# Kernel optimization log

Hardware: AMD Instinct MI355X
Metric: run time of the kernel (lower is better)

## Reference

```python
import jax, jax.numpy as jnp
import numpy as np

N = 100000      # num_nodes
E = 1600000     # num_edges (avg degree 16)
D_IN, D_H, D_OUT = 128, 128, 64


def _glorot(key, shape):
    fan_in = shape[0]
    bound = 1.0 / np.sqrt(fan_in)
    return jax.random.uniform(key, shape, jnp.float32, -bound, bound)


def setup_inputs() -> dict:
    key = jax.random.key(0)
    ks = jax.random.split(key, 9)
    x = jax.random.normal(ks[0], (N, D_IN), jnp.float32)
    edge_index = jax.random.randint(ks[1], (2, E), 0, N, jnp.int32)
    # SAGEConv layer 1: lin_l (aggregated, with bias) and lin_r (root, no bias)
    W1l = _glorot(ks[2], (D_IN, D_H))
    b1 = jnp.zeros((D_H,), jnp.float32)
    W1r = _glorot(ks[3], (D_IN, D_H))
    # SAGEConv layer 2
    W2l = _glorot(ks[4], (D_H, D_OUT))
    b2 = jnp.zeros((D_OUT,), jnp.float32)
    W2r = _glorot(ks[5], (D_H, D_OUT))
    return {"x": x, "W1l": W1l, "b1": b1, "W1r": W1r,
            "W2l": W2l, "b2": b2, "W2r": W2r, "edge_index": edge_index}


def _sage_conv(x, edge_index, Wl, b, Wr):
    """PyG SAGEConv with mean aggregation: out = mean_{j in N(i)} x_j @ Wl + b + x_i @ Wr."""
    src, dst = edge_index[0], edge_index[1]
    msg_sum = jax.ops.segment_sum(x[src], dst, num_segments=N)          # [N, d_in]
    deg = jax.ops.segment_sum(jnp.ones((src.shape[0],), x.dtype), dst,
                              num_segments=N)                            # [N]
    mean = msg_sum / jnp.maximum(deg, 1.0)[:, None]
    return mean @ Wl + b + x @ Wr


def reference(x, W1l, b1, W1r, W2l, b2, W2r, edge_index):
    h = jax.nn.relu(_sage_conv(x, edge_index, W1l, b1, W1r))
    # dropout is identity at inference (training=False)
    return _sage_conv(h, edge_index, W2l, b2, W2r)
```

## Files before the change

kernel.cpp:

```cpp
#include <hip/hip_runtime.h>

#define NODES 100000
#define NEDGE 1600000
#define NPART 8
#define PSIZE (NODES / NPART)
#define EW 48

typedef _Float16 half8 __attribute__((ext_vector_type(8)));
typedef float floatx4 __attribute__((ext_vector_type(4)));
typedef float floatx2 __attribute__((ext_vector_type(2)));


static __device__ __forceinline__ unsigned int packh2(float a, float b) {
    union { _Float16 h; unsigned short s; } x, y;
    x.h = (_Float16)a; y.h = (_Float16)b;
    return (unsigned int)x.s | ((unsigned int)y.s << 16);
}
static __device__ __forceinline__ float2 unpackh2(unsigned int u) {
    union { unsigned short s; _Float16 h; } x, y;
    x.s = (unsigned short)(u & 0xffffu);
    y.s = (unsigned short)(u >> 16);
    return make_float2((float)x.h, (float)y.h);
}


template <bool HI>
static __device__ __forceinline__ float2 fp8x2_to_f32(unsigned int u) {
    floatx2 r = __builtin_amdgcn_cvt_pk_f32_fp8(u, HI);
    return make_float2(r.x, r.y);
}
static __device__ __forceinline__ unsigned int pack4fp8(float a, float b,
                                                        float c, float d) {
    unsigned int w = (unsigned int)__builtin_amdgcn_cvt_pk_fp8_f32(a, b, 0, false);
    w = (unsigned int)__builtin_amdgcn_cvt_pk_fp8_f32(c, d, (int)w, true);
    return w;
}


static __global__ __launch_bounds__(256) void prep_kernel(
    const float* __restrict__ W1l, const float* __restrict__ W1r,
    const float* __restrict__ W2l, const float* __restrict__ W2r,
    _Float16* __restrict__ WT1, _Float16* __restrict__ WT2,
    int* __restrict__ cnt) {
    int bid = blockIdx.x;
    if (bid < 192) {
        int idx = bid * 256 + threadIdx.x;
        if (idx < 256 * 128) {
            int n = idx >> 7, k = idx & 127;
            float v = (n < 128) ? W1l[k * 128 + n] : W1r[k * 128 + (n - 128)];
            WT1[n * 128 + k] = (_Float16)v;
        } else if (idx < 256 * 128 + 128 * 128) {
            int i2 = idx - 256 * 128;
            int n = i2 >> 7, k = i2 & 127;
            float v = (n < 64) ? W2l[k * 64 + n] : W2r[k * 64 + (n - 64)];
            WT2[n * 128 + k] = (_Float16)v;
        }
    } else {
        int i = (bid - 192) * 256 + threadIdx.x;
        int stride = 128 * 256;
        for (; i < NODES; i += stride) cnt[i] = 0;
    }
}


static __global__ __launch_bounds__(256) void build_ell_kernel(
    const int* __restrict__ src, const int* __restrict__ dst,
    int* __restrict__ cnt, int* __restrict__ colE,
    int ebase, int eend) {
    const int part = blockIdx.x & (NPART - 1);
    const int lo = part * PSIZE;
    const int hi = lo + PSIZE;
    const int group = blockIdx.x >> 3;
    const int ngroups = gridDim.x >> 3;
    int i = group * 256 + threadIdx.x;
    int stride = ngroups * 256;
    for (int e = ebase + i; e < eend; e += stride) {
        int d = __builtin_nontemporal_load(dst + e);
        if (d >= lo && d < hi) {
            int sv = __builtin_nontemporal_load(src + e);
            int pos = atomicAdd(&cnt[d], 1);
            if (pos < EW) colE[(size_t)d * EW + pos] = sv;
        }
    }
}


static __global__ __launch_bounds__(256) void gemm1_mfma_kernel(
    const float* __restrict__ X, const _Float16* __restrict__ WT1,
    const float* __restrict__ b1,
    unsigned char* __restrict__ U8, _Float16* __restrict__ V16) {
    __shared__ _Float16 sX[64][136];
    const int tid = threadIdx.x;
    const int row0 = blockIdx.x * 64;
    {
        int c4 = (tid & 31) * 4;
        int r0 = tid >> 5;
#pragma unroll
        for (int p = 0; p < 8; ++p) {
            int r = r0 + p * 8;
            int row = row0 + r;
            float4 v = make_float4(0.f, 0.f, 0.f, 0.f);
            if (row < NODES) v = *(const float4*)(X + (size_t)row * 128 + c4);
            uint2 o;
            o.x = packh2(v.x, v.y);
            o.y = packh2(v.z, v.w);
            *(uint2*)&sX[r][c4] = o;
        }
    }
    __syncthreads();

    const int wave = tid >> 6;
    const int lane = tid & 63;
    const int l15 = lane & 15;
    const int quad = lane >> 4;

    floatx4 acc[4][4];
#pragma unroll
    for (int j = 0; j < 4; ++j)
#pragma unroll
        for (int m = 0; m < 4; ++m) acc[j][m] = (floatx4){0.f, 0.f, 0.f, 0.f};

    const _Float16* Wbase = WT1 + (size_t)(wave * 64 + l15) * 128 + quad * 8;

    for (int k0 = 0; k0 < 128; k0 += 32) {
        half8 a[4];
#pragma unroll
        for (int m = 0; m < 4; ++m)
            a[m] = *(const half8*)&sX[m * 16 + l15][quad * 8 + k0];
#pragma unroll
        for (int j = 0; j < 4; ++j) {
            half8 b = *(const half8*)(Wbase + (size_t)j * 16 * 128 + k0);
#pragma unroll
            for (int m = 0; m < 4; ++m)
                acc[j][m] = __builtin_amdgcn_mfma_f32_16x16x32_f16(b, a[m], acc[j][m], 0, 0, 0);
        }
    }

    if (wave < 2) {
#pragma unroll
        for (int j = 0; j < 4; ++j) {
            int n0 = wave * 64 + j * 16 + quad * 4;
#pragma unroll
            for (int m = 0; m < 4; ++m) {
                int node = row0 + m * 16 + l15;
                if (node < NODES) {
                    unsigned int w = pack4fp8(acc[j][m][0], acc[j][m][1],
                                              acc[j][m][2], acc[j][m][3]);
                    *(unsigned int*)(U8 + (size_t)node * 128 + n0) = w;
                }
            }
        }
    } else {
#pragma unroll
        for (int j = 0; j < 4; ++j) {
            int nn0 = (wave - 2) * 64 + j * 16 + quad * 4;
            float4 bb = *(const float4*)(b1 + nn0);
#pragma unroll
            for (int m = 0; m < 4; ++m) {
                int node = row0 + m * 16 + l15;
                if (node < NODES) {
                    uint2 o;
                    o.x = packh2(acc[j][m][0] + bb.x, acc[j][m][1] + bb.y);
                    o.y = packh2(acc[j][m][2] + bb.z, acc[j][m][3] + bb.w);
                    *(uint2*)(V16 + (size_t)node * 128 + nn0) = o;
                }
            }
        }
    }
}


static __global__ __launch_bounds__(256) void agg1_kernel(
    const unsigned char* __restrict__ U8, const int* __restrict__ cnt,
    const int* __restrict__ colE, unsigned int* __restrict__ H32) {
    int node = (int)((blockIdx.x * 256 + threadIdx.x) >> 6);
    int lane = threadIdx.x & 63;
    if (node >= NODES) return;
    const int g = lane >> 4;
    const int l16 = lane & 15;
    int dcnt = cnt[node];
    if (dcnt > EW) dcnt = EW;
    int s = node * EW;
    int e = s + dcnt;
    float inv = 1.0f / (float)max(dcnt, 1);

    float acc[8];
#pragma unroll
    for (int i = 0; i < 8; ++i) acc[i] = 0.f;

    int p = s + g;
    for (; p + 12 < e; p += 16) {
        int c0 = colE[p], c1 = colE[p + 4], c2 = colE[p + 8], c3 = colE[p + 12];
        uint2 u0 = *(const uint2*)(U8 + (size_t)c0 * 128 + l16 * 8);
        uint2 u1 = *(const uint2*)(U8 + (size_t)c1 * 128 + l16 * 8);
        uint2 u2 = *(const uint2*)(U8 + (size_t)c2 * 128 + l16 * 8);
        uint2 u3 = *(const uint2*)(U8 + (size_t)c3 * 128 + l16 * 8);
#pragma unroll
        for (int q = 0; q < 4; ++q) {
            uint2 u = (q == 0) ? u0 : (q == 1) ? u1 : (q == 2) ? u2 : u3;
            float2 a0 = fp8x2_to_f32<false>(u.x), a1 = fp8x2_to_f32<true>(u.x);
            float2 a2 = fp8x2_to_f32<false>(u.y), a3 = fp8x2_to_f32<true>(u.y);
            acc[0] += a0.x; acc[1] += a0.y; acc[2] += a1.x; acc[3] += a1.y;
            acc[4] += a2.x; acc[5] += a2.y; acc[6] += a3.x; acc[7] += a3.y;
        }
    }
    for (; p < e; p += 4) {
        uint2 u = *(const uint2*)(U8 + (size_t)colE[p] * 128 + l16 * 8);
        float2 a0 = fp8x2_to_f32<false>(u.x), a1 = fp8x2_to_f32<true>(u.x);
        float2 a2 = fp8x2_to_f32<false>(u.y), a3 = fp8x2_to_f32<true>(u.y);
        acc[0] += a0.x; acc[1] += a0.y; acc[2] += a1.x; acc[3] += a1.y;
        acc[4] += a2.x; acc[5] += a2.y; acc[6] += a3.x; acc[7] += a3.y;
    }

#pragma unroll
    for (int i = 0; i < 8; ++i) {
        acc[i] += __shfl_xor(acc[i], 16);
        acc[i] += __shfl_xor(acc[i], 32);
    }

    if (lane < 16) {
        uint4 vv = *(const uint4*)(H32 + (size_t)node * 64 + l16 * 4);
        float2 v0 = unpackh2(vv.x), v1 = unpackh2(vv.y);
        float2 v2 = unpackh2(vv.z), v3 = unpackh2(vv.w);
        uint4 o;
        o.x = packh2(fmaxf(acc[0] * inv + v0.x, 0.f), fmaxf(acc[1] * inv + v0.y, 0.f));
        o.y = packh2(fmaxf(acc[2] * inv + v1.x, 0.f), fmaxf(acc[3] * inv + v1.y, 0.f));
        o.z = packh2(fmaxf(acc[4] * inv + v2.x, 0.f), fmaxf(acc[5] * inv + v2.y, 0.f));
        o.w = packh2(fmaxf(acc[6] * inv + v3.x, 0.f), fmaxf(acc[7] * inv + v3.y, 0.f));
        *(uint4*)(H32 + (size_t)node * 64 + l16 * 4) = o;
    }
}


static __global__ __launch_bounds__(256) void gemm2_mfma_kernel(
    const _Float16* __restrict__ H16, const _Float16* __restrict__ WT2,
    const float* __restrict__ b2,
    _Float16* __restrict__ T16, float* __restrict__ OUT) {
    __shared__ _Float16 sX[64][136];
    const int tid = threadIdx.x;
    const int row0 = blockIdx.x * 64;
    {
        int c8 = (tid & 15) * 8;
        int r0 = tid >> 4;
#pragma unroll
        for (int p = 0; p < 4; ++p) {
            int r = r0 + p * 16;
            int row = row0 + r;
            uint4 v = make_uint4(0u, 0u, 0u, 0u);
            if (row < NODES) v = *(const uint4*)(H16 + (size_t)row * 128 + c8);
            *(uint4*)&sX[r][c8] = v;
        }
    }
    __syncthreads();

    const int wave = tid >> 6;
    const int lane = tid & 63;
    const int l15 = lane & 15;
    const int quad = lane >> 4;

    floatx4 acc[2][4];
#pragma unroll
    for (int j = 0; j < 2; ++j)
#pragma unroll
        for (int m = 0; m < 4; ++m) acc[j][m] = (floatx4){0.f, 0.f, 0.f, 0.f};

    const _Float16* Wbase = WT2 + (size_t)(wave * 32 + l15) * 128 + quad * 8;

    for (int k0 = 0; k0 < 128; k0 += 32) {
        half8 a[4];
#pragma unroll
        for (int m = 0; m < 4; ++m)
            a[m] = *(const half8*)&sX[m * 16 + l15][quad * 8 + k0];
#pragma unroll
        for (int j = 0; j < 2; ++j) {
            half8 b = *(const half8*)(Wbase + (size_t)j * 16 * 128 + k0);
#pragma unroll
            for (int m = 0; m < 4; ++m)
                acc[j][m] = __builtin_amdgcn_mfma_f32_16x16x32_f16(b, a[m], acc[j][m], 0, 0, 0);
        }
    }

    const bool isOut = (wave >= 2);
#pragma unroll
    for (int j = 0; j < 2; ++j) {
        int n0 = wave * 32 + j * 16 + quad * 4;
        if (isOut) {
            int nn0 = n0 - 64;
            float4 bb = *(const float4*)(b2 + nn0);
#pragma unroll
            for (int m = 0; m < 4; ++m) {
                int node = row0 + m * 16 + l15;
                if (node < NODES) {
                    float4 o = make_float4(acc[j][m][0] + bb.x, acc[j][m][1] + bb.y,
                                           acc[j][m][2] + bb.z, acc[j][m][3] + bb.w);
                    *(float4*)(OUT + (size_t)node * 64 + nn0) = o;
                }
            }
        } else {
#pragma unroll
            for (int m = 0; m < 4; ++m) {
                int node = row0 + m * 16 + l15;
                if (node < NODES) {
                    uint2 o;
                    o.x = packh2(acc[j][m][0], acc[j][m][1]);
                    o.y = packh2(acc[j][m][2], acc[j][m][3]);
                    *(uint2*)(T16 + (size_t)node * 64 + n0) = o;
                }
            }
        }
    }
}


static __global__ __launch_bounds__(256) void agg2_kernel(
    const unsigned int* __restrict__ T32, const int* __restrict__ cnt,
    const int* __restrict__ colE, float* __restrict__ OUT) {
    int node = (int)((blockIdx.x * 256 + threadIdx.x) >> 6);
    int lane = threadIdx.x & 63;
    if (node >= NODES) return;
    const int g = lane >> 4;
    const int l16 = lane & 15;
    int dcnt = cnt[node];
    if (dcnt > EW) dcnt = EW;
    int s = node * EW;
    int e = s + dcnt;
    float inv = 1.0f / (float)max(dcnt, 1);

    float acc[4];
#pragma unroll
    for (int i = 0; i < 4; ++i) acc[i] = 0.f;

    int p = s + g;
    for (; p + 12 < e; p += 16) {
        int c0 = colE[p], c1 = colE[p + 4], c2 = colE[p + 8], c3 = colE[p + 12];
        uint2 u0 = *(const uint2*)(T32 + (size_t)c0 * 32 + l16 * 2);
        uint2 u1 = *(const uint2*)(T32 + (size_t)c1 * 32 + l16 * 2);
        uint2 u2 = *(const uint2*)(T32 + (size_t)c2 * 32 + l16 * 2);
        uint2 u3 = *(const uint2*)(T32 + (size_t)c3 * 32 + l16 * 2);
#pragma unroll
        for (int q = 0; q < 4; ++q) {
            uint2 u = (q == 0) ? u0 : (q == 1) ? u1 : (q == 2) ? u2 : u3;
            float2 a0 = unpackh2(u.x), a1 = unpackh2(u.y);
            acc[0] += a0.x; acc[1] += a0.y; acc[2] += a1.x; acc[3] += a1.y;
        }
    }
    for (; p < e; p += 4) {
        uint2 u = *(const uint2*)(T32 + (size_t)colE[p] * 32 + l16 * 2);
        float2 a0 = unpackh2(u.x), a1 = unpackh2(u.y);
        acc[0] += a0.x; acc[1] += a0.y; acc[2] += a1.x; acc[3] += a1.y;
    }

#pragma unroll
    for (int i = 0; i < 4; ++i) {
        acc[i] += __shfl_xor(acc[i], 16);
        acc[i] += __shfl_xor(acc[i], 32);
    }

    if (lane < 16) {
        float4 o = *(float4*)(OUT + (size_t)node * 64 + l16 * 4);
        o.x += acc[0] * inv;
        o.y += acc[1] * inv;
        o.z += acc[2] * inv;
        o.w += acc[3] * inv;
        *(float4*)(OUT + (size_t)node * 64 + l16 * 4) = o;
    }
}


extern "C" void kernel_launch(void* const* d_in, const int* in_sizes, int n_in,
                              void* d_out, int out_size, void* d_ws, size_t ws_size,
                              hipStream_t stream) {
    const float* x   = (const float*)d_in[0];
    const float* W1l = (const float*)d_in[1];
    const float* b1  = (const float*)d_in[2];
    const float* W1r = (const float*)d_in[3];
    const float* W2l = (const float*)d_in[4];
    const float* b2  = (const float*)d_in[5];
    const float* W2r = (const float*)d_in[6];
    const int*   ei  = (const int*)d_in[7];
    const int* esrc = ei;
    const int* edst = ei + NEDGE;
    float* out = (float*)d_out;

    char* ws = (char*)d_ws;
    size_t off = 0;
    int* colE     = (int*)(ws + off); off += (size_t)NODES * EW * 4;
    unsigned char* U8 = (unsigned char*)(ws + off); off += (size_t)NODES * 128;
    _Float16* V16 = (_Float16*)(ws + off); off += (size_t)NODES * 128 * 2;
    int* cnt      = (int*)(ws + off); off += (((size_t)NODES * 4) + 255) & ~(size_t)255;
    _Float16* WT1 = (_Float16*)(ws + off); off += 256 * 128 * 2;
    _Float16* WT2 = (_Float16*)(ws + off); off += 128 * 128 * 2;
    _Float16* T16 = (_Float16*)U8;

    const int gemm_grid = (NODES + 63) / 64;
    const int agg_grid  = (NODES + 3) / 4;

    prep_kernel<<<320, 256, 0, stream>>>(W1l, W1r, W2l, W2r, WT1, WT2, cnt);
    build_ell_kernel<<<1024, 256, 0, stream>>>(esrc, edst, cnt, colE,
                                               0, NEDGE / 2);
    build_ell_kernel<<<1024, 256, 0, stream>>>(esrc, edst, cnt, colE,
                                               NEDGE / 2, NEDGE);

    gemm1_mfma_kernel<<<gemm_grid, 256, 0, stream>>>(x, WT1, b1, U8, V16);
    agg1_kernel<<<agg_grid, 256, 0, stream>>>(U8, cnt, colE, (unsigned int*)V16);

    gemm2_mfma_kernel<<<gemm_grid, 256, 0, stream>>>(V16, WT2, b2, T16, out);
    agg2_kernel<<<agg_grid, 256, 0, stream>>>(
        (const unsigned int*)T16, cnt, colE, out);
}
```

Baseline: 372.0 us.

## Fuse layer-1 aggregation into layer-2 GEMM and merge ELL build launches

Layer-1 mean aggregation (with root add and ReLU) now runs inside the layer-2 MFMA GEMM block. Each wave aggregates 16 nodes straight into shared memory instead of writing H to global and reading it back. T16 is written into the V16 buffer with a 128-half stride, and agg2 indexing is updated to match. The two half-range ELL build launches become a single 2048-block launch. Fusing drops one global round trip and one launch, but each GEMM block now serialises 16 gather loops per wave, which lowers memory-level parallelism compared with one wave per node across the whole grid.

```diff
diff --git a/kernel.cpp b/kernel.cpp
--- a/kernel.cpp
+++ b/kernel.cpp
@@ -65,8 +65,7 @@
 
 static __global__ __launch_bounds__(256) void build_ell_kernel(
     const int* __restrict__ src, const int* __restrict__ dst,
-    int* __restrict__ cnt, int* __restrict__ colE,
-    int ebase, int eend) {
+    int* __restrict__ cnt, int* __restrict__ colE) {
     const int part = blockIdx.x & (NPART - 1);
     const int lo = part * PSIZE;
     const int hi = lo + PSIZE;
@@ -74,7 +73,7 @@
     const int ngroups = gridDim.x >> 3;
     int i = group * 256 + threadIdx.x;
     int stride = ngroups * 256;
-    for (int e = ebase + i; e < eend; e += stride) {
+    for (int e = i; e < NEDGE; e += stride) {
         int d = __builtin_nontemporal_load(dst + e);
         if (d >= lo && d < hi) {
             int sv = __builtin_nontemporal_load(src + e);
@@ -170,99 +169,86 @@
 }
 
 
-static __global__ __launch_bounds__(256) void agg1_kernel(
+static __global__ __launch_bounds__(256) void agg1_gemm2_kernel(
     const unsigned char* __restrict__ U8, const int* __restrict__ cnt,
-    const int* __restrict__ colE, unsigned int* __restrict__ H32) {
-    int node = (int)((blockIdx.x * 256 + threadIdx.x) >> 6);
-    int lane = threadIdx.x & 63;
-    if (node >= NODES) return;
-    const int g = lane >> 4;
-    const int l16 = lane & 15;
-    int dcnt = cnt[node];
-    if (dcnt > EW) dcnt = EW;
-    int s = node * EW;
-    int e = s + dcnt;
-    float inv = 1.0f / (float)max(dcnt, 1);
-
-    float acc[8];
-#pragma unroll
-    for (int i = 0; i < 8; ++i) acc[i] = 0.f;
-
-    int p = s + g;
-    for (; p + 12 < e; p += 16) {
-        int c0 = colE[p], c1 = colE[p + 4], c2 = colE[p + 8], c3 = colE[p + 12];
-        uint2 u0 = *(const uint2*)(U8 + (size_t)c0 * 128 + l16 * 8);
-        uint2 u1 = *(const uint2*)(U8 + (size_t)c1 * 128 + l16 * 8);
-        uint2 u2 = *(const uint2*)(U8 + (size_t)c2 * 128 + l16 * 8);
-        uint2 u3 = *(const uint2*)(U8 + (size_t)c3 * 128 + l16 * 8);
-#pragma unroll
-        for (int q = 0; q < 4; ++q) {
-            uint2 u = (q == 0) ? u0 : (q == 1) ? u1 : (q == 2) ? u2 : u3;
-            float2 a0 = fp8x2_to_f32<false>(u.x), a1 = fp8x2_to_f32<true>(u.x);
-            float2 a2 = fp8x2_to_f32<false>(u.y), a3 = fp8x2_to_f32<true>(u.y);
-            acc[0] += a0.x; acc[1] += a0.y; acc[2] += a1.x; acc[3] += a1.y;
-            acc[4] += a2.x; acc[5] += a2.y; acc[6] += a3.x; acc[7] += a3.y;
-        }
-    }
-    for (; p < e; p += 4) {
-        uint2 u = *(const uint2*)(U8 + (size_t)colE[p] * 128 + l16 * 8);
-        float2 a0 = fp8x2_to_f32<false>(u.x), a1 = fp8x2_to_f32<true>(u.x);
-        float2 a2 = fp8x2_to_f32<false>(u.y), a3 = fp8x2_to_f32<true>(u.y);
-        acc[0] += a0.x; acc[1] += a0.y; acc[2] += a1.x; acc[3] += a1.y;
-        acc[4] += a2.x; acc[5] += a2.y; acc[6] += a3.x; acc[7] += a3.y;
-    }
-
-#pragma unroll
-    for (int i = 0; i < 8; ++i) {
-        acc[i] += __shfl_xor(acc[i], 16);
-        acc[i] += __shfl_xor(acc[i], 32);
-    }
-
-    if (lane < 16) {
-        uint4 vv = *(const uint4*)(H32 + (size_t)node * 64 + l16 * 4);
-        float2 v0 = unpackh2(vv.x), v1 = unpackh2(vv.y);
-        float2 v2 = unpackh2(vv.z), v3 = unpackh2(vv.w);
-        uint4 o;
-        o.x = packh2(fmaxf(acc[0] * inv + v0.x, 0.f), fmaxf(acc[1] * inv + v0.y, 0.f));
-        o.y = packh2(fmaxf(acc[2] * inv + v1.x, 0.f), fmaxf(acc[3] * inv + v1.y, 0.f));
-        o.z = packh2(fmaxf(acc[4] * inv + v2.x, 0.f), fmaxf(acc[5] * inv + v2.y, 0.f));
-        o.w = packh2(fmaxf(acc[6] * inv + v3.x, 0.f), fmaxf(acc[7] * inv + v3.y, 0.f));
-        *(uint4*)(H32 + (size_t)node * 64 + l16 * 4) = o;
-    }
-}
-
-
-static __global__ __launch_bounds__(256) void gemm2_mfma_kernel(
-    const _Float16* __restrict__ H16, const _Float16* __restrict__ WT2,
-    const float* __restrict__ b2,
-    _Float16* __restrict__ T16, float* __restrict__ OUT) {
+    const int* __restrict__ colE, const _Float16* __restrict__ WT2,
+    const float* __restrict__ b2, _Float16* __restrict__ V16,
+    float* __restrict__ OUT) {
     __shared__ _Float16 sX[64][136];
     const int tid = threadIdx.x;
     const int row0 = blockIdx.x * 64;
-    {
-        int c8 = (tid & 15) * 8;
-        int r0 = tid >> 4;
-#pragma unroll
-        for (int p = 0; p < 4; ++p) {
-            int r = r0 + p * 16;
-            int row = row0 + r;
-            uint4 v = make_uint4(0u, 0u, 0u, 0u);
-            if (row < NODES) v = *(const uint4*)(H16 + (size_t)row * 128 + c8);
-            *(uint4*)&sX[r][c8] = v;
-        }
-    }
-    __syncthreads();
-
     const int wave = tid >> 6;
     const int lane = tid & 63;
+    const int g = lane >> 4;
+    const int l16 = lane & 15;
+    const unsigned int* H32 = (const unsigned int*)V16;
+
+    for (int m = 0; m < 16; ++m) {
+        const int r = wave * 16 + m;
+        const int node = row0 + r;
+        float acc[8];
+#pragma unroll
+        for (int i = 0; i < 8; ++i) acc[i] = 0.f;
+        float inv = 1.0f;
+        if (node < NODES) {
+            int dcnt = cnt[node];
+            if (dcnt > EW) dcnt = EW;
+            int s = node * EW;
+            int e = s + dcnt;
+            inv = 1.0f / (float)max(dcnt, 1);
+            int p = s + g;
+            for (; p + 12 < e; p += 16) {
+                int c0 = colE[p], c1 = colE[p + 4], c2 = colE[p + 8], c3 = colE[p + 12];
+                uint2 u0 = *(const uint2*)(U8 + (size_t)c0 * 128 + l16 * 8);
+                uint2 u1 = *(const uint2*)(U8 + (size_t)c1 * 128 + l16 * 8);
+                uint2 u2 = *(const uint2*)(U8 + (size_t)c2 * 128 + l16 * 8);
+                uint2 u3 = *(const uint2*)(U8 + (size_t)c3 * 128 + l16 * 8);
+#pragma unroll
+                for (int q = 0; q < 4; ++q) {
+                    uint2 u = (q == 0) ? u0 : (q == 1) ? u1 : (q == 2) ? u2 : u3;
+                    float2 a0 = fp8x2_to_f32<false>(u.x), a1 = fp8x2_to_f32<true>(u.x);
+                    float2 a2 = fp8x2_to_f32<false>(u.y), a3 = fp8x2_to_f32<true>(u.y);
+                    acc[0] += a0.x; acc[1] += a0.y; acc[2] += a1.x; acc[3] += a1.y;
+                    acc[4] += a2.x; acc[5] += a2.y; acc[6] += a3.x; acc[7] += a3.y;
+                }
+            }
+            for (; p < e; p += 4) {
+                uint2 u = *(const uint2*)(U8 + (size_t)colE[p] * 128 + l16 * 8);
+                float2 a0 = fp8x2_to_f32<false>(u.x), a1 = fp8x2_to_f32<true>(u.x);
+                float2 a2 = fp8x2_to_f32<false>(u.y), a3 = fp8x2_to_f32<true>(u.y);
+                acc[0] += a0.x; acc[1] += a0.y; acc[2] += a1.x; acc[3] += a1.y;
+                acc[4] += a2.x; acc[5] += a2.y; acc[6] += a3.x; acc[7] += a3.y;
+            }
+        }
+#pragma unroll
+        for (int i = 0; i < 8; ++i) {
+            acc[i] += __shfl_xor(acc[i], 16);
+            acc[i] += __shfl_xor(acc[i], 32);
+        }
+        if (lane < 16) {
+            uint4 o = make_uint4(0u, 0u, 0u, 0u);
+            if (node < NODES) {
+                uint4 vv = *(const uint4*)(H32 + (size_t)node * 64 + l16 * 4);
+                float2 v0 = unpackh2(vv.x), v1 = unpackh2(vv.y);
+                float2 v2 = unpackh2(vv.z), v3 = unpackh2(vv.w);
+                o.x = packh2(fmaxf(acc[0] * inv + v0.x, 0.f), fmaxf(acc[1] * inv + v0.y, 0.f));
+                o.y = packh2(fmaxf(acc[2] * inv + v1.x, 0.f), fmaxf(acc[3] * inv + v1.y, 0.f));
+                o.z = packh2(fmaxf(acc[4] * inv + v2.x, 0.f), fmaxf(acc[5] * inv + v2.y, 0.f));
+                o.w = packh2(fmaxf(acc[6] * inv + v3.x, 0.f), fmaxf(acc[7] * inv + v3.y, 0.f));
+            }
+            *(uint4*)&sX[r][l16 * 8] = o;
+        }
+    }
+    __syncthreads();
+
     const int l15 = lane & 15;
     const int quad = lane >> 4;
 
-    floatx4 acc[2][4];
+    floatx4 acc2[2][4];
 #pragma unroll
     for (int j = 0; j < 2; ++j)
 #pragma unroll
-        for (int m = 0; m < 4; ++m) acc[j][m] = (floatx4){0.f, 0.f, 0.f, 0.f};
+        for (int m = 0; m < 4; ++m) acc2[j][m] = (floatx4){0.f, 0.f, 0.f, 0.f};
 
     const _Float16* Wbase = WT2 + (size_t)(wave * 32 + l15) * 128 + quad * 8;
 
@@ -276,7 +262,7 @@
             half8 b = *(const half8*)(Wbase + (size_t)j * 16 * 128 + k0);
 #pragma unroll
             for (int m = 0; m < 4; ++m)
-                acc[j][m] = __builtin_amdgcn_mfma_f32_16x16x32_f16(b, a[m], acc[j][m], 0, 0, 0);
+                acc2[j][m] = __builtin_amdgcn_mfma_f32_16x16x32_f16(b, a[m], acc2[j][m], 0, 0, 0);
         }
     }
 
@@ -291,8 +277,8 @@
             for (int m = 0; m < 4; ++m) {
                 int node = row0 + m * 16 + l15;
                 if (node < NODES) {
-                    float4 o = make_float4(acc[j][m][0] + bb.x, acc[j][m][1] + bb.y,
-                                           acc[j][m][2] + bb.z, acc[j][m][3] + bb.w);
+                    float4 o = make_float4(acc2[j][m][0] + bb.x, acc2[j][m][1] + bb.y,
+                                           acc2[j][m][2] + bb.z, acc2[j][m][3] + bb.w);
                     *(float4*)(OUT + (size_t)node * 64 + nn0) = o;
                 }
             }
@@ -302,9 +288,9 @@
                 int node = row0 + m * 16 + l15;
                 if (node < NODES) {
                     uint2 o;
-                    o.x = packh2(acc[j][m][0], acc[j][m][1]);
-                    o.y = packh2(acc[j][m][2], acc[j][m][3]);
-                    *(uint2*)(T16 + (size_t)node * 64 + n0) = o;
+                    o.x = packh2(acc2[j][m][0], acc2[j][m][1]);
+                    o.y = packh2(acc2[j][m][2], acc2[j][m][3]);
+                    *(uint2*)(V16 + (size_t)node * 128 + n0) = o;
                 }
             }
         }
@@ -333,10 +319,10 @@
     int p = s + g;
     for (; p + 12 < e; p += 16) {
         int c0 = colE[p], c1 = colE[p + 4], c2 = colE[p + 8], c3 = colE[p + 12];
-        uint2 u0 = *(const uint2*)(T32 + (size_t)c0 * 32 + l16 * 2);
-        uint2 u1 = *(const uint2*)(T32 + (size_t)c1 * 32 + l16 * 2);
-        uint2 u2 = *(const uint2*)(T32 + (size_t)c2 * 32 + l16 * 2);
-        uint2 u3 = *(const uint2*)(T32 + (size_t)c3 * 32 + l16 * 2);
+        uint2 u0 = *(const uint2*)(T32 + (size_t)c0 * 64 + l16 * 2);
+        uint2 u1 = *(const uint2*)(T32 + (size_t)c1 * 64 + l16 * 2);
+        uint2 u2 = *(const uint2*)(T32 + (size_t)c2 * 64 + l16 * 2);
+        uint2 u3 = *(const uint2*)(T32 + (size_t)c3 * 64 + l16 * 2);
 #pragma unroll
         for (int q = 0; q < 4; ++q) {
             uint2 u = (q == 0) ? u0 : (q == 1) ? u1 : (q == 2) ? u2 : u3;
@@ -345,7 +331,7 @@
         }
     }
     for (; p < e; p += 4) {
-        uint2 u = *(const uint2*)(T32 + (size_t)colE[p] * 32 + l16 * 2);
+        uint2 u = *(const uint2*)(T32 + (size_t)colE[p] * 64 + l16 * 2);
         float2 a0 = unpackh2(u.x), a1 = unpackh2(u.y);
         acc[0] += a0.x; acc[1] += a0.y; acc[2] += a1.x; acc[3] += a1.y;
     }
@@ -390,21 +376,18 @@
     int* cnt      = (int*)(ws + off); off += (((size_t)NODES * 4) + 255) & ~(size_t)255;
     _Float16* WT1 = (_Float16*)(ws + off); off += 256 * 128 * 2;
     _Float16* WT2 = (_Float16*)(ws + off); off += 128 * 128 * 2;
-    _Float16* T16 = (_Float16*)U8;
 
     const int gemm_grid = (NODES + 63) / 64;
     const int agg_grid  = (NODES + 3) / 4;
 
     prep_kernel<<<320, 256, 0, stream>>>(W1l, W1r, W2l, W2r, WT1, WT2, cnt);
-    build_ell_kernel<<<1024, 256, 0, stream>>>(esrc, edst, cnt, colE,
-                                               0, NEDGE / 2);
-    build_ell_kernel<<<1024, 256, 0, stream>>>(esrc, edst, cnt, colE,
-                                               NEDGE / 2, NEDGE);
+    build_ell_kernel<<<2048, 256, 0, stream>>>(esrc, edst, cnt, colE);
 
     gemm1_mfma_kernel<<<gemm_grid, 256, 0, stream>>>(x, WT1, b1, U8, V16);
-    agg1_kernel<<<agg_grid, 256, 0, stream>>>(U8, cnt, colE, (unsigned int*)V16);
-
-    gemm2_mfma_kernel<<<gemm_grid, 256, 0, stream>>>(V16, WT2, b2, T16, out);
+
+    agg1_gemm2_kernel<<<gemm_grid, 256, 0, stream>>>(U8, cnt, colE, WT2, b2,
+                                                     V16, out);
+
     agg2_kernel<<<agg_grid, 256, 0, stream>>>(
-        (const unsigned int*)T16, cnt, colE, out);
-}
+        (const unsigned int*)V16, cnt, colE, out);
+}
```

Result: no change. 378.2 us (+1.7%).

## Process two nodes per wavefront in aggregation and merge ELL build launches

Applied to the files above, without the earlier changes.

Both aggregation kernels now give each 64-lane wavefront two destination nodes. Each iteration issues eight predicated gathers, four per node, with masked loads replacing the remainder loop, so more memory requests are in flight per wave. The ELL build collapses two half-range launches into a single launch with twice the blocks, removing one kernel launch. The cost is more registers per thread, wasted lanes when the two nodes' degrees differ, and a dummy row-0 load for each invalid slot.

```diff
diff --git a/kernel.cpp b/kernel.cpp
--- a/kernel.cpp
+++ b/kernel.cpp
@@ -65,8 +65,7 @@
 
 static __global__ __launch_bounds__(256) void build_ell_kernel(
     const int* __restrict__ src, const int* __restrict__ dst,
-    int* __restrict__ cnt, int* __restrict__ colE,
-    int ebase, int eend) {
+    int* __restrict__ cnt, int* __restrict__ colE) {
     const int part = blockIdx.x & (NPART - 1);
     const int lo = part * PSIZE;
     const int hi = lo + PSIZE;
@@ -74,7 +73,7 @@
     const int ngroups = gridDim.x >> 3;
     int i = group * 256 + threadIdx.x;
     int stride = ngroups * 256;
-    for (int e = ebase + i; e < eend; e += stride) {
+    for (int e = i; e < NEDGE; e += stride) {
         int d = __builtin_nontemporal_load(dst + e);
         if (d >= lo && d < hi) {
             int sv = __builtin_nontemporal_load(src + e);
@@ -173,61 +172,100 @@
 static __global__ __launch_bounds__(256) void agg1_kernel(
     const unsigned char* __restrict__ U8, const int* __restrict__ cnt,
     const int* __restrict__ colE, unsigned int* __restrict__ H32) {
-    int node = (int)((blockIdx.x * 256 + threadIdx.x) >> 6);
+    int pid = (int)((blockIdx.x * 256 + threadIdx.x) >> 6);
     int lane = threadIdx.x & 63;
-    if (node >= NODES) return;
+    const int nA = pid * 2;
+    const int nB = nA + 1;
+    if (nA >= NODES) return;
     const int g = lane >> 4;
     const int l16 = lane & 15;
-    int dcnt = cnt[node];
-    if (dcnt > EW) dcnt = EW;
-    int s = node * EW;
-    int e = s + dcnt;
-    float inv = 1.0f / (float)max(dcnt, 1);
-
-    float acc[8];
-#pragma unroll
-    for (int i = 0; i < 8; ++i) acc[i] = 0.f;
-
-    int p = s + g;
-    for (; p + 12 < e; p += 16) {
-        int c0 = colE[p], c1 = colE[p + 4], c2 = colE[p + 8], c3 = colE[p + 12];
-        uint2 u0 = *(const uint2*)(U8 + (size_t)c0 * 128 + l16 * 8);
-        uint2 u1 = *(const uint2*)(U8 + (size_t)c1 * 128 + l16 * 8);
-        uint2 u2 = *(const uint2*)(U8 + (size_t)c2 * 128 + l16 * 8);
-        uint2 u3 = *(const uint2*)(U8 + (size_t)c3 * 128 + l16 * 8);
+
+    int dA = cnt[nA]; if (dA > EW) dA = EW;
+    int dB = (nB < NODES) ? cnt[nB] : 0; if (dB > EW) dB = EW;
+    const int sA = nA * EW, sB = nB * EW;
+    const int eA = sA + dA, eB = sB + dB;
+    const float invA = 1.0f / (float)max(dA, 1);
+    const float invB = 1.0f / (float)max(dB, 1);
+    const int dmax = max(dA, dB);
+
+    float accA[8], accB[8];
+#pragma unroll
+    for (int i = 0; i < 8; ++i) { accA[i] = 0.f; accB[i] = 0.f; }
+
+    for (int t = 0; t * 16 < dmax; ++t) {
+        int bA = sA + g + t * 16, bB = sB + g + t * 16;
+        int pA0 = bA, pA1 = bA + 4, pA2 = bA + 8, pA3 = bA + 12;
+        int pB0 = bB, pB1 = bB + 4, pB2 = bB + 8, pB3 = bB + 12;
+        bool vA0 = pA0 < eA, vA1 = pA1 < eA, vA2 = pA2 < eA, vA3 = pA3 < eA;
+        bool vB0 = pB0 < eB, vB1 = pB1 < eB, vB2 = pB2 < eB, vB3 = pB3 < eB;
+        int cA0 = colE[vA0 ? pA0 : sA], cA1 = colE[vA1 ? pA1 : sA];
+        int cA2 = colE[vA2 ? pA2 : sA], cA3 = colE[vA3 ? pA3 : sA];
+        int cB0 = colE[vB0 ? pB0 : sB], cB1 = colE[vB1 ? pB1 : sB];
+        int cB2 = colE[vB2 ? pB2 : sB], cB3 = colE[vB3 ? pB3 : sB];
+        cA0 = vA0 ? cA0 : 0; cA1 = vA1 ? cA1 : 0;
+        cA2 = vA2 ? cA2 : 0; cA3 = vA3 ? cA3 : 0;
+        cB0 = vB0 ? cB0 : 0; cB1 = vB1 ? cB1 : 0;
+        cB2 = vB2 ? cB2 : 0; cB3 = vB3 ? cB3 : 0;
+        uint2 uA0 = *(const uint2*)(U8 + (size_t)cA0 * 128 + l16 * 8);
+        uint2 uA1 = *(const uint2*)(U8 + (size_t)cA1 * 128 + l16 * 8);
+        uint2 uA2 = *(const uint2*)(U8 + (size_t)cA2 * 128 + l16 * 8);
+        uint2 uA3 = *(const uint2*)(U8 + (size_t)cA3 * 128 + l16 * 8);
+        uint2 uB0 = *(const uint2*)(U8 + (size_t)cB0 * 128 + l16 * 8);
+        uint2 uB1 = *(const uint2*)(U8 + (size_t)cB1 * 128 + l16 * 8);
+        uint2 uB2 = *(const uint2*)(U8 + (size_t)cB2 * 128 + l16 * 8);
+        uint2 uB3 = *(const uint2*)(U8 + (size_t)cB3 * 128 + l16 * 8);
+        if (!vA0) { uA0.x = 0u; uA0.y = 0u; }
+        if (!vA1) { uA1.x = 0u; uA1.y = 0u; }
+        if (!vA2) { uA2.x = 0u; uA2.y = 0u; }
+        if (!vA3) { uA3.x = 0u; uA3.y = 0u; }
+        if (!vB0) { uB0.x = 0u; uB0.y = 0u; }
+        if (!vB1) { uB1.x = 0u; uB1.y = 0u; }
+        if (!vB2) { uB2.x = 0u; uB2.y = 0u; }
+        if (!vB3) { uB3.x = 0u; uB3.y = 0u; }
 #pragma unroll
         for (int q = 0; q < 4; ++q) {
-            uint2 u = (q == 0) ? u0 : (q == 1) ? u1 : (q == 2) ? u2 : u3;
+            uint2 u = (q == 0) ? uA0 : (q == 1) ? uA1 : (q == 2) ? uA2 : uA3;
             float2 a0 = fp8x2_to_f32<false>(u.x), a1 = fp8x2_to_f32<true>(u.x);
             float2 a2 = fp8x2_to_f32<false>(u.y), a3 = fp8x2_to_f32<true>(u.y);
-            acc[0] += a0.x; acc[1] += a0.y; acc[2] += a1.x; acc[3] += a1.y;
-            acc[4] += a2.x; acc[5] += a2.y; acc[6] += a3.x; acc[7] += a3.y;
-        }
-    }
-    for (; p < e; p += 4) {
-        uint2 u = *(const uint2*)(U8 + (size_t)colE[p] * 128 + l16 * 8);
-        float2 a0 = fp8x2_to_f32<false>(u.x), a1 = fp8x2_to_f32<true>(u.x);
-        float2 a2 = fp8x2_to_f32<false>(u.y), a3 = fp8x2_to_f32<true>(u.y);
-        acc[0] += a0.x; acc[1] += a0.y; acc[2] += a1.x; acc[3] += a1.y;
-        acc[4] += a2.x; acc[5] += a2.y; acc[6] += a3.x; acc[7] += a3.y;
+            accA[0] += a0.x; accA[1] += a0.y; accA[2] += a1.x; accA[3] += a1.y;
+            accA[4] += a2.x; accA[5] += a2.y; accA[6] += a3.x; accA[7] += a3.y;
+        }
+#pragma unroll
+        for (int q = 0; q < 4; ++q) {
+            uint2 u = (q == 0) ? uB0 : (q == 1) ? uB1 : (q == 2) ? uB2 : uB3;
+            float2 a0 = fp8x2_to_f32<false>(u.x), a1 = fp8x2_to_f32<true>(u.x);
+            float2 a2 = fp8x2_to_f32<false>(u.y), a3 = fp8x2_to_f32<true>(u.y);
+            accB[0] += a0.x; accB[1] += a0.y; accB[2] += a1.x; accB[3] += a1.y;
+            accB[4] += a2.x; accB[5] += a2.y; accB[6] += a3.x; accB[7] += a3.y;
+        }
     }
 
 #pragma unroll
     for (int i = 0; i < 8; ++i) {
-        acc[i] += __shfl_xor(acc[i], 16);
-        acc[i] += __shfl_xor(acc[i], 32);
-    }
-
-    if (lane < 16) {
-        uint4 vv = *(const uint4*)(H32 + (size_t)node * 64 + l16 * 4);
-        float2 v0 = unpackh2(vv.x), v1 = unpackh2(vv.y);
-        float2 v2 = unpackh2(vv.z), v3 = unpackh2(vv.w);
-        uint4 o;
-        o.x = packh2(fmaxf(acc[0] * inv + v0.x, 0.f), fmaxf(acc[1] * inv + v0.y, 0.f));
-        o.y = packh2(fmaxf(acc[2] * inv + v1.x, 0.f), fmaxf(acc[3] * inv + v1.y, 0.f));
-        o.z = packh2(fmaxf(acc[4] * inv + v2.x, 0.f), fmaxf(acc[5] * inv + v2.y, 0.f));
-        o.w = packh2(fmaxf(acc[6] * inv + v3.x, 0.f), fmaxf(acc[7] * inv + v3.y, 0.f));
-        *(uint4*)(H32 + (size_t)node * 64 + l16 * 4) = o;
+        accA[i] += __shfl_xor(accA[i], 16);
+        accA[i] += __shfl_xor(accA[i], 32);
+        accB[i] += __shfl_xor(accB[i], 16);
+        accB[i] += __shfl_xor(accB[i], 32);
+    }
+
+    if (lane < 32) {
+        const bool isA = lane < 16;
+        const int node = isA ? nA : nB;
+        if (node < NODES) {
+            const float inv = isA ? invA : invB;
+            float r[8];
+#pragma unroll
+            for (int i = 0; i < 8; ++i) r[i] = isA ? accA[i] : accB[i];
+            uint4 vv = *(const uint4*)(H32 + (size_t)node * 64 + l16 * 4);
+            float2 v0 = unpackh2(vv.x), v1 = unpackh2(vv.y);
+            float2 v2 = unpackh2(vv.z), v3 = unpackh2(vv.w);
+            uint4 o;
+            o.x = packh2(fmaxf(r[0] * inv + v0.x, 0.f), fmaxf(r[1] * inv + v0.y, 0.f));
+            o.y = packh2(fmaxf(r[2] * inv + v1.x, 0.f), fmaxf(r[3] * inv + v1.y, 0.f));
+            o.z = packh2(fmaxf(r[4] * inv + v2.x, 0.f), fmaxf(r[5] * inv + v2.y, 0.f));
+            o.w = packh2(fmaxf(r[6] * inv + v3.x, 0.f), fmaxf(r[7] * inv + v3.y, 0.f));
+            *(uint4*)(H32 + (size_t)node * 64 + l16 * 4) = o;
+        }
     }
 }
 
@@ -315,54 +353,94 @@
 static __global__ __launch_bounds__(256) void agg2_kernel(
     const unsigned int* __restrict__ T32, const int* __restrict__ cnt,
     const int* __restrict__ colE, float* __restrict__ OUT) {
-    int node = (int)((blockIdx.x * 256 + threadIdx.x) >> 6);
+    int pid = (int)((blockIdx.x * 256 + threadIdx.x) >> 6);
     int lane = threadIdx.x & 63;
-    if (node >= NODES) return;
+    const int nA = pid * 2;
+    const int nB = nA + 1;
+    if (nA >= NODES) return;
     const int g = lane >> 4;
     const int l16 = lane & 15;
-    int dcnt = cnt[node];
-    if (dcnt > EW) dcnt = EW;
-    int s = node * EW;
-    int e = s + dcnt;
-    float inv = 1.0f / (float)max(dcnt, 1);
-
-    float acc[4];
-#pragma unroll
-    for (int i = 0; i < 4; ++i) acc[i] = 0.f;
-
-    int p = s + g;
-    for (; p + 12 < e; p += 16) {
-        int c0 = colE[p], c1 = colE[p + 4], c2 = colE[p + 8], c3 = colE[p + 12];
-        uint2 u0 = *(const uint2*)(T32 + (size_t)c0 * 32 + l16 * 2);
-        uint2 u1 = *(const uint2*)(T32 + (size_t)c1 * 32 + l16 * 2);
-        uint2 u2 = *(const uint2*)(T32 + (size_t)c2 * 32 + l16 * 2);
-        uint2 u3 = *(const uint2*)(T32 + (size_t)c3 * 32 + l16 * 2);
+
+    int dA = cnt[nA]; if (dA > EW) dA = EW;
+    int dB = (nB < NODES) ? cnt[nB] : 0; if (dB > EW) dB = EW;
+    const int sA = nA * EW, sB = nB * EW;
+    const int eA = sA + dA, eB = sB + dB;
+    const float invA = 1.0f / (float)max(dA, 1);
+    const float invB = 1.0f / (float)max(dB, 1);
+    const int dmax = max(dA, dB);
+
+    float accA[4], accB[4];
+#pragma unroll
+    for (int i = 0; i < 4; ++i) { accA[i] = 0.f; accB[i] = 0.f; }
+
+    for (int t = 0; t * 16 < dmax; ++t) {
+        int bA = sA + g + t * 16, bB = sB + g + t * 16;
+        int pA0 = bA, pA1 = bA + 4, pA2 = bA + 8, pA3 = bA + 12;
+        int pB0 = bB, pB1 = bB + 4, pB2 = bB + 8, pB3 = bB + 12;
+        bool vA0 = pA0 < eA, vA1 = pA1 < eA, vA2 = pA2 < eA, vA3 = pA3 < eA;
+        bool vB0 = pB0 < eB, vB1 = pB1 < eB, vB2 = pB2 < eB, vB3 = pB3 < eB;
+        int cA0 = colE[vA0 ? pA0 : sA], cA1 = colE[vA1 ? pA1 : sA];
+        int cA2 = colE[vA2 ? pA2 : sA], cA3 = colE[vA3 ? pA3 : sA];
+        int cB0 = colE[vB0 ? pB0 : sB], cB1 = colE[vB1 ? pB1 : sB];
+        int cB2 = colE[vB2 ? pB2 : sB], cB3 = colE[vB3 ? pB3 : sB];
+        cA0 = vA0 ? cA0 : 0; cA1 = vA1 ? cA1 : 0;
+        cA2 = vA2 ? cA2 : 0; cA3 = vA3 ? cA3 : 0;
+        cB0 = vB0 ? cB0 : 0; cB1 = vB1 ? cB1 : 0;
+        cB2 = vB2 ? cB2 : 0; cB3 = vB3 ? cB3 : 0;
+        uint2 uA0 = *(const uint2*)(T32 + (size_t)cA0 * 32 + l16 * 2);
+        uint2 uA1 = *(const uint2*)(T32 + (size_t)cA1 * 32 + l16 * 2);
+        uint2 uA2 = *(const uint2*)(T32 + (size_t)cA2 * 32 + l16 * 2);
+        uint2 uA3 = *(const uint2*)(T32 + (size_t)cA3 * 32 + l16 * 2);
+        uint2 uB0 = *(const uint2*)(T32 + (size_t)cB0 * 32 + l16 * 2);
+        uint2 uB1 = *(const uint2*)(T32 + (size_t)cB1 * 32 + l16 * 2);
+        uint2 uB2 = *(const uint2*)(T32 + (size_t)cB2 * 32 + l16 * 2);
+        uint2 uB3 = *(const uint2*)(T32 + (size_t)cB3 * 32 + l16 * 2);
+        if (!vA0) { uA0.x = 0u; uA0.y = 0u; }
+        if (!vA1) { uA1.x = 0u; uA1.y = 0u; }
+        if (!vA2) { uA2.x = 0u; uA2.y = 0u; }
+        if (!vA3) { uA3.x = 0u; uA3.y = 0u; }
+        if (!vB0) { uB0.x = 0u; uB0.y = 0u; }
+        if (!vB1) { uB1.x = 0u; uB1.y = 0u; }
+        if (!vB2) { uB2.x = 0u; uB2.y = 0u; }
+        if (!vB3) { uB3.x = 0u; uB3.y = 0u; }
 #pragma unroll
         for (int q = 0; q < 4; ++q) {
-            uint2 u = (q == 0) ? u0 : (q == 1) ? u1 : (q == 2) ? u2 : u3;
+            uint2 u = (q == 0) ? uA0 : (q == 1) ? uA1 : (q == 2) ? uA2 : uA3;
             float2 a0 = unpackh2(u.x), a1 = unpackh2(u.y);
-            acc[0] += a0.x; acc[1] += a0.y; acc[2] += a1.x; acc[3] += a1.y;
-        }
-    }
-    for (; p < e; p += 4) {
-        uint2 u = *(const uint2*)(T32 + (size_t)colE[p] * 32 + l16 * 2);
-        float2 a0 = unpackh2(u.x), a1 = unpackh2(u.y);
-        acc[0] += a0.x; acc[1] += a0.y; acc[2] += a1.x; acc[3] += a1.y;
+            accA[0] += a0.x; accA[1] += a0.y; accA[2] += a1.x; accA[3] += a1.y;
+        }
+#pragma unroll
+        for (int q = 0; q < 4; ++q) {
+            uint2 u = (q == 0) ? uB0 : (q == 1) ? uB1 : (q == 2) ? uB2 : uB3;
+            float2 a0 = unpackh2(u.x), a1 = unpackh2(u.y);
+            accB[0] += a0.x; accB[1] += a0.y; accB[2] += a1.x; accB[3] += a1.y;
+        }
     }
 
 #pragma unroll
     for (int i = 0; i < 4; ++i) {
-        acc[i] += __shfl_xor(acc[i], 16);
-        acc[i] += __shfl_xor(acc[i], 32);
-    }
-
-    if (lane < 16) {
-        float4 o = *(float4*)(OUT + (size_t)node * 64 + l16 * 4);
-        o.x += acc[0] * inv;
-        o.y += acc[1] * inv;
-        o.z += acc[2] * inv;
-        o.w += acc[3] * inv;
-        *(float4*)(OUT + (size_t)node * 64 + l16 * 4) = o;
+        accA[i] += __shfl_xor(accA[i], 16);
+        accA[i] += __shfl_xor(accA[i], 32);
+        accB[i] += __shfl_xor(accB[i], 16);
+        accB[i] += __shfl_xor(accB[i], 32);
+    }
+
+    if (lane < 32) {
+        const bool isA = lane < 16;
+        const int node = isA ? nA : nB;
+        if (node < NODES) {
+            const float inv = isA ? invA : invB;
+            float r0 = isA ? accA[0] : accB[0];
+            float r1 = isA ? accA[1] : accB[1];
+            float r2 = isA ? accA[2] : accB[2];
+            float r3 = isA ? accA[3] : accB[3];
+            float4 o = *(float4*)(OUT + (size_t)node * 64 + l16 * 4);
+            o.x += r0 * inv;
+            o.y += r1 * inv;
+            o.z += r2 * inv;
+            o.w += r3 * inv;
+            *(float4*)(OUT + (size_t)node * 64 + l16 * 4) = o;
+        }
     }
 }
 
@@ -393,13 +471,11 @@
     _Float16* T16 = (_Float16*)U8;
 
     const int gemm_grid = (NODES + 63) / 64;
-    const int agg_grid  = (NODES + 3) / 4;
+    const int npairs = (NODES + 1) / 2;
+    const int agg_grid = (npairs + 3) / 4;
 
     prep_kernel<<<320, 256, 0, stream>>>(W1l, W1r, W2l, W2r, WT1, WT2, cnt);
-    build_ell_kernel<<<1024, 256, 0, stream>>>(esrc, edst, cnt, colE,
-                                               0, NEDGE / 2);
-    build_ell_kernel<<<1024, 256, 0, stream>>>(esrc, edst, cnt, colE,
-                                               NEDGE / 2, NEDGE);
+    build_ell_kernel<<<2048, 256, 0, stream>>>(esrc, edst, cnt, colE);
 
     gemm1_mfma_kernel<<<gemm_grid, 256, 0, stream>>>(x, WT1, b1, U8, V16);
     agg1_kernel<<<agg_grid, 256, 0, stream>>>(U8, cnt, colE, (unsigned int*)V16);
```

After: 303.0 us. 1.23x faster.
